# Optimization experiments

Hardware: AMD Instinct MI355X
Metric: run time of the kernel (lower is better)

The kernel has to match this reference:

```python
import jax, jax.numpy as jnp
import numpy as np

B, S = 4, 1024          # 4 prefill sequences of length 1024 (cu_seqlens equal-length)
D_MODEL = 2048
N_HEADS = 32
N_KV_HEADS = 8
HEAD_DIM = D_MODEL // N_HEADS          # 64
GROUPS = N_HEADS // N_KV_HEADS         # 4
ROPE_THETA = 10000.0
SCALE = HEAD_DIM ** -0.5


def setup_inputs() -> dict:
    key = jax.random.key(0)
    ks = jax.random.split(key, 6)
    T = B * S
    hidden_states = jax.random.normal(ks[0], (T, D_MODEL), jnp.float32)
    # rotary tables: positions restart per sequence (prefill)
    pos = jnp.tile(jnp.arange(S, dtype=jnp.float32), B)            # [T]
    inv_freq = 1.0 / (ROPE_THETA ** (jnp.arange(0, HEAD_DIM, 2, dtype=jnp.float32) / HEAD_DIM))
    freqs = pos[:, None] * inv_freq[None, :]                        # [T, HEAD_DIM/2]
    cos, sin = jnp.cos(freqs), jnp.sin(freqs)
    std = D_MODEL ** -0.5
    Wq = jax.random.normal(ks[1], (D_MODEL, N_HEADS * HEAD_DIM), jnp.float32) * std
    Wk = jax.random.normal(ks[2], (D_MODEL, N_KV_HEADS * HEAD_DIM), jnp.float32) * std
    Wv = jax.random.normal(ks[3], (D_MODEL, N_KV_HEADS * HEAD_DIM), jnp.float32) * std
    Wo = jax.random.normal(ks[4], (N_HEADS * HEAD_DIM, D_MODEL), jnp.float32) * std
    return {"hidden_states": hidden_states, "cos": cos, "sin": sin,
            "Wq": Wq, "Wk": Wk, "Wv": Wv, "Wo": Wo}


def _rope(x, cos, sin):
    # NeoX-style rotary: x [T, H, D], cos/sin [T, D/2]
    half = x.shape[-1] // 2
    x1, x2 = x[..., :half], x[..., half:]
    c, s = cos[:, None, :], sin[:, None, :]
    return jnp.concatenate([x1 * c - x2 * s, x2 * c + x1 * s], axis=-1)


def reference(hidden_states, cos, sin, Wq, Wk, Wv, Wo):
    T = hidden_states.shape[0]
    q = (hidden_states @ Wq).reshape(T, N_HEADS, HEAD_DIM)
    k = (hidden_states @ Wk).reshape(T, N_KV_HEADS, HEAD_DIM)
    v = (hidden_states @ Wv).reshape(T, N_KV_HEADS, HEAD_DIM)
    q = _rope(q, cos, sin)
    k = _rope(k, cos, sin)
    # equal-length varlen prefill -> [B, S, H, D]
    q = q.reshape(B, S, N_HEADS, HEAD_DIM)
    k = jnp.repeat(k.reshape(B, S, N_KV_HEADS, HEAD_DIM), GROUPS, axis=2)  # GQA expand
    v = jnp.repeat(v.reshape(B, S, N_KV_HEADS, HEAD_DIM), GROUPS, axis=2)
    scores = jnp.einsum("bqhd,bkhd->bhqk", q, k) * SCALE
    causal = jnp.tril(jnp.ones((S, S), dtype=bool))
    scores = jnp.where(causal[None, None], scores, jnp.finfo(scores.dtype).min)
    probs = jax.nn.softmax(scores, axis=-1)
    attn = jnp.einsum("bhqk,bkhd->bqhd", probs, v).reshape(T, N_HEADS * HEAD_DIM)
    return attn @ Wo
```

## Files before the change

kernel.cpp:

```cpp
#include <hip/hip_runtime.h>
#include <type_traits>


typedef __bf16 bf16x8 __attribute__((ext_vector_type(8)));
typedef __bf16 bf16x4 __attribute__((ext_vector_type(4)));
typedef float f32x4 __attribute__((ext_vector_type(4)));
typedef unsigned short u16;
typedef unsigned int u32;

#define DEVI __device__ __forceinline__

DEVI u16 f2bf(float f) {
  u32 u = __builtin_bit_cast(u32, f);
  u += 0x7FFF + ((u >> 16) & 1);
  return (u16)(u >> 16);
}

DEVI void ld16_lds(const void* g, void* l) {
  __builtin_amdgcn_global_load_lds((const __attribute__((address_space(1))) u32*)g,
                                   (__attribute__((address_space(3))) u32*)l, 16, 0, 0);
}

template <int N> DEVI void waitvm() {
  if constexpr (N == 0) asm volatile("s_waitcnt vmcnt(0)" ::: "memory");
  else if constexpr (N == 3) asm volatile("s_waitcnt vmcnt(3)" ::: "memory");
  else if constexpr (N == 4) asm volatile("s_waitcnt vmcnt(4)" ::: "memory");
  else static_assert(N == 0, "unsupported vmcnt");
}
DEVI void lgkm0() {
  asm volatile("s_waitcnt lgkmcnt(0)" ::: "memory");
  __builtin_amdgcn_sched_barrier(0);
}
DEVI void barrier() { __builtin_amdgcn_s_barrier(); }

__global__ __launch_bounds__(256) void convert_f32_bf16(const float* __restrict__ src,
                                                        u16* __restrict__ dst, int n4) {
  int i = blockIdx.x * 256 + threadIdx.x;
  if (i >= n4) return;
  float4 v = ((const float4*)src)[i];
  ushort4 o;
  o.x = f2bf(v.x); o.y = f2bf(v.y); o.z = f2bf(v.z); o.w = f2bf(v.w);
  ((ushort4*)dst)[i] = o;
}

__global__ __launch_bounds__(256) void trans_f32_bf16(const float* __restrict__ src,
                                                      u16* __restrict__ dst, int R, int C,
                                                      float scale) {
  __shared__ float tile[32][33];
  int c0 = blockIdx.x * 32, r0 = blockIdx.y * 32;
  int tx = threadIdx.x & 31, ty = threadIdx.x >> 5;
#pragma unroll
  for (int i = 0; i < 32; i += 8)
    tile[ty + i][tx] = src[(size_t)(r0 + ty + i) * C + (c0 + tx)];
  __syncthreads();
#pragma unroll
  for (int i = 0; i < 32; i += 8)
    dst[(size_t)(c0 + ty + i) * R + (r0 + tx)] = f2bf(tile[tx][ty + i] * scale);
}

template <typename OutT, bool ROPE, int BN>
__global__ __launch_bounds__(512, 2) void gemm8(const u16* __restrict__ A,
                                                const u16* __restrict__ BT,
                                                OutT* __restrict__ C, int M, int N, int K,
                                                const float* __restrict__ cs,
                                                const float* __restrict__ sn) {
  constexpr int WN = BN / 64;
  constexpr int NH = WN / 2;
  constexpr int LB = BN / 128;
  constexpr int VMP = 2 + LB;
  __shared__ u16 As[2][256 * 64];
  __shared__ u16 Bs[2][BN * 64];
  const int tid = threadIdx.x;
  const int lane = tid & 63, wave = tid >> 6;
  const int quad = lane >> 4, l16 = lane & 15;
  const int m0 = blockIdx.y * 256, n0 = blockIdx.x * BN;
  const int wr = wave >> 2, wc = wave & 3;

  f32x4 acc[8][WN] = {};

  auto stageA = [&](int t, int h) {
    u16* D = &As[t & 1][h * 8192];
    const u16* G = A + (size_t)m0 * K + t * 64;
#pragma unroll
    for (int i = 0; i < 2; ++i) {
      int id = i * 512 + tid;
      int row = h * 128 + (id >> 3), ch = id & 7;
      ld16_lds(G + (size_t)row * K + (ch ^ (row & 7)) * 8, D + id * 8);
    }
  };
  auto stageB = [&](int t, int h) {
    u16* D = &Bs[t & 1][h * (BN / 2) * 64];
    const u16* G = BT + (size_t)n0 * K + t * 64;
#pragma unroll
    for (int i = 0; i < LB; ++i) {
      int id = i * 512 + tid;
      int row = h * (BN / 2) + (id >> 3), ch = id & 7;
      ld16_lds(G + (size_t)row * K + (ch ^ (row & 7)) * 8, D + id * 8);
    }
  };

  bf16x8 af[4][2], bv0[NH][2], bv1[NH][2];
  auto ldA = [&](int msub, int d) {
#pragma unroll
    for (int i = 0; i < 4; ++i)
#pragma unroll
      for (int ks = 0; ks < 2; ++ks) {
        int r = wr * 128 + msub * 64 + i * 16 + l16;
        af[i][ks] = *(const bf16x8*)&As[d][r * 64 + (((ks * 4 + quad) ^ (r & 7)) * 8)];
      }
  };
  auto ldB = [&](bf16x8 (&bv)[NH][2], int nsub, int d) {
#pragma unroll
    for (int j = 0; j < NH; ++j)
#pragma unroll
      for (int ks = 0; ks < 2; ++ks) {
        int rb = wc * (16 * WN) + (nsub * NH + j) * 16 + l16;
        bv[j][ks] = *(const bf16x8*)&Bs[d][rb * 64 + (((ks * 4 + quad) ^ (rb & 7)) * 8)];
      }
  };
  auto mm = [&](const bf16x8 (&bv)[NH][2], int mo, int no) {
    __builtin_amdgcn_s_setprio(1);
#pragma unroll
    for (int i = 0; i < 4; ++i)
#pragma unroll
      for (int j = 0; j < NH; ++j)
#pragma unroll
        for (int ks = 0; ks < 2; ++ks)
          acc[mo + i][no + j] =
              __builtin_amdgcn_mfma_f32_16x16x32_bf16(af[i][ks], bv[j][ks], acc[mo + i][no + j], 0, 0, 0);
    __builtin_amdgcn_s_setprio(0);
  };

  const int NT = K / 64;

  stageA(0, 0); stageA(0, 1); stageB(0, 0); stageB(0, 1);
  stageB(1, 0); stageA(1, 0);
  waitvm<VMP>();
  barrier();

#pragma unroll 1
  for (int T = 0; T < NT; T += 2) {
    const bool pf = (T + 2 < NT);
    ldA(0, 0); ldB(bv0, 0, 0);
    stageA(T + 1, 1);
    barrier(); lgkm0();
    mm(bv0, 0, 0);
    barrier();

    ldB(bv1, 1, 0);
    stageB(T + 1, 1);
    barrier(); lgkm0();
    mm(bv1, 0, NH);
    barrier();

    ldA(1, 0);
    if (pf) stageB(T + 2, 0);
    barrier(); lgkm0();
    mm(bv1, 4, NH);
    barrier();

    if (pf) { stageA(T + 2, 0); waitvm<VMP>(); }
    else waitvm<0>();
    barrier();
    __builtin_amdgcn_sched_barrier(0);
    mm(bv0, 4, 0);
    barrier();

    ldA(0, 1); ldB(bv0, 0, 1);
    if (pf) stageB(T + 2, 1);
    barrier(); lgkm0();
    mm(bv0, 0, 0);
    barrier();

    ldB(bv1, 1, 1);
    if (pf) stageA(T + 2, 1);
    barrier(); lgkm0();
    mm(bv1, 0, NH);
    barrier();

    ldA(1, 1);
    if (pf) stageB(T + 3, 0);
    barrier(); lgkm0();
    mm(bv1, 4, NH);
    barrier();

    if (pf) {
      stageA(T + 3, 0);
      waitvm<VMP>();
      barrier();
      __builtin_amdgcn_sched_barrier(0);
      mm(bv0, 4, 0);
      barrier();
    } else {
      mm(bv0, 4, 0);
    }
  }

  if constexpr (ROPE) {
    if (n0 + wc * (16 * WN) < 2560) {
#pragma unroll
      for (int i = 0; i < 8; i++) {
        int t0 = m0 + wr * 128 + i * 16 + quad * 4;
#pragma unroll
        for (int jj = 0; jj < 2; jj++) {
          int d = jj * 16 + l16;
#pragma unroll
          for (int r = 0; r < 4; r++) {
            float cv = cs[(size_t)(t0 + r) * 32 + d];
            float sv = sn[(size_t)(t0 + r) * 32 + d];
            float x1 = acc[i][jj][r], x2 = acc[i][jj + 2][r];
            acc[i][jj][r] = x1 * cv - x2 * sv;
            acc[i][jj + 2][r] = x2 * cv + x1 * sv;
          }
        }
      }
    }
  }

#pragma unroll
  for (int i = 0; i < 8; i++) {
    int row = m0 + wr * 128 + i * 16 + quad * 4;
#pragma unroll
    for (int j = 0; j < WN; j++) {
      int col = n0 + wc * (16 * WN) + j * 16 + l16;
#pragma unroll
      for (int r = 0; r < 4; r++) {
        size_t off = (size_t)(row + r) * N + col;
        if constexpr (sizeof(OutT) == 2) C[off] = f2bf(acc[i][j][r]);
        else C[off] = acc[i][j][r];
      }
    }
  }
}

__global__ __launch_bounds__(256) void vkt_build(const u16* __restrict__ qkv,
                                                 u16* __restrict__ vkt) {
  __shared__ u16 Vn[128 * 64];
  const int kt = blockIdx.x, kvh = blockIdx.y, b = blockIdx.z;
  const int tid = threadIdx.x;
  const u16* src = qkv + ((size_t)b * 1024 + kt * 128) * 3072 + 2560 + kvh * 64;
  {
    int tok = tid >> 1, hf = tid & 1;
    const uint4* s4 = (const uint4*)(src + (size_t)tok * 3072 + hf * 32);
    uint4* d4 = (uint4*)&Vn[tok * 64 + hf * 32];
#pragma unroll
    for (int j = 0; j < 4; j++) d4[j] = s4[j];
  }
  __syncthreads();
  u16* img = vkt + ((((size_t)b * 8 + kvh) * 8 + kt) << 13);
#pragma unroll
  for (int i = 0; i < 4; i++) {
    int c = tid * 4 + i;
    int dd = c >> 4, chsw = c & 15;
    int ch = chsw ^ (dd & 15);
    u16 tmp[8];
#pragma unroll
    for (int p = 0; p < 8; p++) {
      int col = ch * 8 + p;
      int g = col >> 5, kl = col & 31;
      int kph = ((kl >> 2) & 1) * 16 + ((kl >> 4) & 1) * 8 + ((kl >> 3) & 1) * 4 + (kl & 3);
      tmp[p] = Vn[(g * 32 + kph) * 64 + dd];
    }
    *(uint4*)&img[c * 8] = *(const uint4*)tmp;
  }
}

__global__ __launch_bounds__(256, 2) void flash_attn(const u16* __restrict__ qkv,
                                                     const u16* __restrict__ vkt,
                                                     u16* __restrict__ attn) {
  __shared__ u16 Ks[2][128 * 64];
  __shared__ u16 VT[2][64 * 128];

  const int tid = threadIdx.x;
  const int lane = tid & 63, wave = tid >> 6;
  const int quad = lane >> 4, l16 = lane & 15;
  const int qtA = blockIdx.x, qtB = 7 - blockIdx.x;
  const int h = blockIdx.y, b = blockIdx.z, kvh = h >> 2;
  const size_t tokBase = (size_t)b * 1024;
  const int qcol = h * 64, kcol = 2048 + kvh * 64;
  const int srow = tid >> 3, spc = tid & 7, ssc = spc ^ (srow & 7);

  auto stageK = [&](const u16* gbase, u16* L) {
#pragma unroll
    for (int i = 0; i < 4; i++)
      ld16_lds(gbase + (size_t)(srow + i * 32) * 3072 + ssc * 8, &L[tid * 8 + i * 2048]);
  };
  const u16* vimg = vkt + (((size_t)b * 8 + kvh) << 16);
  auto stageV = [&](int kt, u16* L) {
    const u16* g = vimg + ((size_t)kt << 13);
#pragma unroll
    for (int i = 0; i < 4; i++)
      ld16_lds(g + i * 2048 + tid * 8, &L[tid * 8 + i * 2048]);
  };

  stageK(qkv + (tokBase + qtA * 128) * 3072 + qcol, Ks[0]);
  stageK(qkv + (tokBase + qtB * 128) * 3072 + qcol, Ks[1]);
  __syncthreads();
  bf16x8 qfA[2][2], qfB[2][2];
#pragma unroll
  for (int nq = 0; nq < 2; nq++) {
    int qrow = wave * 32 + nq * 16 + l16;
#pragma unroll
    for (int ks = 0; ks < 2; ks++) {
      int c = (ks * 4 + quad) ^ (qrow & 7);
      qfA[nq][ks] = *(const bf16x8*)&Ks[0][qrow * 64 + c * 8];
      qfB[nq][ks] = *(const bf16x8*)&Ks[1][qrow * 64 + c * 8];
    }
  }
  __syncthreads();

  float lA[2] = {0.f, 0.f}, lB[2] = {0.f, 0.f};
  f32x4 oA[4][2] = {}, oB[4][2] = {};

  auto proc = [&](const bf16x8 (&kf)[2][2], const bf16x8 (&va)[4], const bf16x8 (&qf)[2][2],
                  f32x4 (&o)[4][2], float (&lacc)[2], bool msk, int c) {
    f32x4 s[2][2] = {};
#pragma unroll
    for (int mkl = 0; mkl < 2; mkl++)
#pragma unroll
      for (int ks = 0; ks < 2; ks++) {
        s[0][mkl] = __builtin_amdgcn_mfma_f32_16x16x32_bf16(kf[mkl][ks], qf[0][ks], s[0][mkl], 0, 0, 0);
        s[1][mkl] = __builtin_amdgcn_mfma_f32_16x16x32_bf16(kf[mkl][ks], qf[1][ks], s[1][mkl], 0, 0, 0);
      }
    if (msk) {
#pragma unroll
      for (int nq = 0; nq < 2; nq++) {
        int q = wave * 32 + nq * 16 + l16;
#pragma unroll
        for (int mkl = 0; mkl < 2; mkl++)
#pragma unroll
          for (int r = 0; r < 4; r++)
            if ((c * 2 + mkl) * 16 + quad * 4 + r > q) s[nq][mkl][r] = -3e38f;
      }
    }
    bf16x8 pf[2];
#pragma unroll
    for (int nq = 0; nq < 2; nq++) {
      float a0 = 0.f;
#pragma unroll
      for (int mkl = 0; mkl < 2; mkl++)
#pragma unroll
        for (int r = 0; r < 4; r++) {
          float p = __builtin_amdgcn_exp2f(s[nq][mkl][r]);
          s[nq][mkl][r] = p;
          a0 += p;
        }
      lacc[nq] += a0;
      pf[nq][0] = (__bf16)s[nq][0][0]; pf[nq][1] = (__bf16)s[nq][0][1];
      pf[nq][2] = (__bf16)s[nq][0][2]; pf[nq][3] = (__bf16)s[nq][0][3];
      pf[nq][4] = (__bf16)s[nq][1][0]; pf[nq][5] = (__bf16)s[nq][1][1];
      pf[nq][6] = (__bf16)s[nq][1][2]; pf[nq][7] = (__bf16)s[nq][1][3];
    }
#pragma unroll
    for (int md = 0; md < 4; md++) {
      o[md][0] = __builtin_amdgcn_mfma_f32_16x16x32_bf16(va[md], pf[0], o[md][0], 0, 0, 0);
      o[md][1] = __builtin_amdgcn_mfma_f32_16x16x32_bf16(va[md], pf[1], o[md][1], 0, 0, 0);
    }
  };

  stageK(qkv + tokBase * 3072 + kcol, Ks[0]);
  stageV(0, VT[0]);

  for (int kt = 0; kt <= qtB; kt++) {
    const int cur = kt & 1;
    __syncthreads();
    if (kt < qtB) {
      stageK(qkv + (tokBase + (kt + 1) * 128) * 3072 + kcol, Ks[1 - cur]);
      stageV(kt + 1, VT[1 - cur]);
    }
    const bool doA = (kt <= qtA), mA = (kt == qtA), mB = (kt == qtB);
    const u16* K = Ks[cur];
    const u16* V = VT[cur];
#pragma unroll
    for (int c = 0; c < 4; c++) {
      bf16x8 kf[2][2];
#pragma unroll
      for (int mkl = 0; mkl < 2; mkl++) {
        int krow = (c * 2 + mkl) * 16 + l16;
#pragma unroll
        for (int ks = 0; ks < 2; ks++)
          kf[mkl][ks] = *(const bf16x8*)&K[krow * 64 + ((ks * 4 + quad) ^ (krow & 7)) * 8];
      }
      bf16x8 va[4];
#pragma unroll
      for (int md = 0; md < 4; md++) {
        int dd = md * 16 + l16;
        va[md] = *(const bf16x8*)&V[dd * 128 + ((c * 4 + quad) ^ l16) * 8];
      }
      proc(kf, va, qfB, oB, lB, mB, c);
      if (doA) proc(kf, va, qfA, oA, lA, mA, c);
    }
  }

  auto epilogue = [&](const f32x4 (&o)[4][2], const float (&lacc)[2], int qt_tile) {
#pragma unroll
    for (int nq = 0; nq < 2; nq++) {
      float l = lacc[nq];
      l += __shfl_xor(l, 16);
      l += __shfl_xor(l, 32);
      float inv = 1.0f / l;
      int t = qt_tile * 128 + wave * 32 + nq * 16 + l16;
      size_t rowOff = (tokBase + t) * 2048 + qcol;
#pragma unroll
      for (int md = 0; md < 4; md++) {
        bf16x4 w;
        w[0] = (__bf16)(o[md][nq][0] * inv);
        w[1] = (__bf16)(o[md][nq][1] * inv);
        w[2] = (__bf16)(o[md][nq][2] * inv);
        w[3] = (__bf16)(o[md][nq][3] * inv);
        *(bf16x4*)&attn[rowOff + md * 16 + quad * 4] = w;
      }
    }
  };
  epilogue(oB, lB, qtB);
  epilogue(oA, lA, qtA);
}

extern "C" void kernel_launch(void* const* d_in, const int* in_sizes, int n_in,
                              void* d_out, int out_size, void* d_ws, size_t ws_size,
                              hipStream_t stream) {
  const float* hs = (const float*)d_in[0];
  const float* cs = (const float*)d_in[1];
  const float* sn = (const float*)d_in[2];
  const float* Wq = (const float*)d_in[3];
  const float* Wk = (const float*)d_in[4];
  const float* Wv = (const float*)d_in[5];
  const float* Wo = (const float*)d_in[6];
  float* out = (float*)d_out;

  char* ws = (char*)d_ws;
  u16* hsB   = (u16*)(ws);
  u16* vkt   = (u16*)(ws);
  u16* wqkvT = (u16*)(ws + 16777216);
  u16* woT   = (u16*)(ws + 29360128);
  u16* qkv   = (u16*)(ws + 37748736);
  u16* attnB = (u16*)(ws + 62914560);

  const float QSCALE = 0.18033688011112042f;

  convert_f32_bf16<<<8192, 256, 0, stream>>>(hs, hsB, 4096 * 2048 / 4);
  trans_f32_bf16<<<dim3(64, 64), 256, 0, stream>>>(Wq, wqkvT, 2048, 2048, QSCALE);
  trans_f32_bf16<<<dim3(16, 64), 256, 0, stream>>>(Wk, wqkvT + (size_t)2048 * 2048, 2048, 512, 1.0f);
  trans_f32_bf16<<<dim3(16, 64), 256, 0, stream>>>(Wv, wqkvT + (size_t)2560 * 2048, 2048, 512, 1.0f);
  trans_f32_bf16<<<dim3(64, 64), 256, 0, stream>>>(Wo, woT, 2048, 2048, 1.0f);

  gemm8<u16, true, 256><<<dim3(12, 16), 512, 0, stream>>>(
      hsB, wqkvT, qkv, 4096, 3072, 2048, cs, sn);
  vkt_build<<<dim3(8, 8, 4), 256, 0, stream>>>(qkv, vkt);
  flash_attn<<<dim3(4, 32, 4), 256, 0, stream>>>(qkv, vkt, attnB);
  gemm8<float, false, 128><<<dim3(16, 16), 512, 0, stream>>>(
      attnB, woT, out, 4096, 2048, 2048, nullptr, nullptr);
}
```

Baseline: 276.8 us.

## Restructure GEMM prefetch into whole-tile stages and swizzle workgroup order

The GEMM main loop now issues loads for full A and B tiles in bursts at a single point each half-iteration, instead of interleaving half-tile stages across phases. It prefetches two full tiles up front and waits with larger vmcnt thresholds. It also remaps block IDs with an XCD-style swizzle, grouping every eighth block so that neighbouring tiles share L2. The aim is simpler load scheduling and better cache locality. The cost is burstier memory traffic and possible hazards if the double-buffer reuse timing no longer matches the new wait points.

```diff
diff --git a/kernel.cpp b/kernel.cpp
--- a/kernel.cpp
+++ b/kernel.cpp
@@ -23,8 +23,8 @@
 
 template <int N> DEVI void waitvm() {
   if constexpr (N == 0) asm volatile("s_waitcnt vmcnt(0)" ::: "memory");
-  else if constexpr (N == 3) asm volatile("s_waitcnt vmcnt(3)" ::: "memory");
-  else if constexpr (N == 4) asm volatile("s_waitcnt vmcnt(4)" ::: "memory");
+  else if constexpr (N == 6) asm volatile("s_waitcnt vmcnt(6)" ::: "memory");
+  else if constexpr (N == 8) asm volatile("s_waitcnt vmcnt(8)" ::: "memory");
   else static_assert(N == 0, "unsupported vmcnt");
 }
 DEVI void lgkm0() {
@@ -67,13 +67,17 @@
   constexpr int WN = BN / 64;
   constexpr int NH = WN / 2;
   constexpr int LB = BN / 128;
-  constexpr int VMP = 2 + LB;
+  constexpr int VMW = 4 + 2 * LB;
   __shared__ u16 As[2][256 * 64];
   __shared__ u16 Bs[2][BN * 64];
   const int tid = threadIdx.x;
   const int lane = tid & 63, wave = tid >> 6;
   const int quad = lane >> 4, l16 = lane & 15;
-  const int m0 = blockIdx.y * 256, n0 = blockIdx.x * BN;
+
+  const int nwg = gridDim.x * gridDim.y;
+  const int bid = blockIdx.y * gridDim.x + blockIdx.x;
+  const int swz = (bid & 7) * (nwg >> 3) + (bid >> 3);
+  const int m0 = (swz / gridDim.x) * 256, n0 = (swz % gridDim.x) * BN;
   const int wr = wave >> 2, wc = wave & 3;
 
   f32x4 acc[8][WN] = {};
@@ -134,59 +138,59 @@
   const int NT = K / 64;
 
   stageA(0, 0); stageA(0, 1); stageB(0, 0); stageB(0, 1);
-  stageB(1, 0); stageA(1, 0);
-  waitvm<VMP>();
+  stageA(1, 0); stageA(1, 1); stageB(1, 0); stageB(1, 1);
+  waitvm<VMW>();
   barrier();
 
 #pragma unroll 1
   for (int T = 0; T < NT; T += 2) {
     const bool pf = (T + 2 < NT);
     ldA(0, 0); ldB(bv0, 0, 0);
-    stageA(T + 1, 1);
     barrier(); lgkm0();
     mm(bv0, 0, 0);
     barrier();
 
     ldB(bv1, 1, 0);
-    stageB(T + 1, 1);
     barrier(); lgkm0();
     mm(bv1, 0, NH);
     barrier();
 
     ldA(1, 0);
-    if (pf) stageB(T + 2, 0);
+    if (pf) { stageB(T + 2, 0); stageB(T + 2, 1); }
     barrier(); lgkm0();
     mm(bv1, 4, NH);
     barrier();
 
-    if (pf) { stageA(T + 2, 0); waitvm<VMP>(); }
-    else waitvm<0>();
+    if (pf) {
+      stageA(T + 2, 0); stageA(T + 2, 1);
+      waitvm<VMW>();
+    } else {
+      waitvm<0>();
+    }
     barrier();
     __builtin_amdgcn_sched_barrier(0);
     mm(bv0, 4, 0);
     barrier();
 
     ldA(0, 1); ldB(bv0, 0, 1);
-    if (pf) stageB(T + 2, 1);
     barrier(); lgkm0();
     mm(bv0, 0, 0);
     barrier();
 
     ldB(bv1, 1, 1);
-    if (pf) stageA(T + 2, 1);
     barrier(); lgkm0();
     mm(bv1, 0, NH);
     barrier();
 
     ldA(1, 1);
-    if (pf) stageB(T + 3, 0);
+    if (pf) { stageB(T + 3, 0); stageB(T + 3, 1); }
     barrier(); lgkm0();
     mm(bv1, 4, NH);
     barrier();
 
     if (pf) {
-      stageA(T + 3, 0);
-      waitvm<VMP>();
+      stageA(T + 3, 0); stageA(T + 3, 1);
+      waitvm<VMW>();
       barrier();
       __builtin_amdgcn_sched_barrier(0);
       mm(bv0, 4, 0);
```

Result: faster. 268.3 us (-3.1%).
